# Performance work log

Hardware: AMD Instinct MI355X
Metric: run time of the kernel (lower is better)

## Reference

```python
import jax, jax.numpy as jnp
import numpy as np

D_MODEL = 1024
NUM_HEADS = 16
HEAD_DIM = D_MODEL // NUM_HEADS


def setup_inputs() -> dict:
    key = jax.random.key(0)
    k_x, k_qw, k_qb, k_pw, k_pb = jax.random.split(key, 5)
    x = jax.random.normal(k_x, (2, 2048, D_MODEL), dtype=jnp.float32)
    s = 1.0 / np.sqrt(D_MODEL)
    qkv_w = jax.random.uniform(k_qw, (3 * D_MODEL, D_MODEL), jnp.float32, -s, s)
    qkv_b = jax.random.uniform(k_qb, (3 * D_MODEL,), jnp.float32, -s, s)
    proj_w = jax.random.uniform(k_pw, (D_MODEL, D_MODEL), jnp.float32, -s, s)
    proj_b = jax.random.uniform(k_pb, (D_MODEL,), jnp.float32, -s, s)
    return {"x": x, "qkv_w": qkv_w, "qkv_b": qkv_b, "proj_w": proj_w, "proj_b": proj_b}


def reference(x, qkv_w, qkv_b, proj_w, proj_b):
    B, N, D = x.shape
    H, hd = NUM_HEADS, HEAD_DIM
    qkv = x @ qkv_w.T + qkv_b                     # [B, N, 3D]
    qkv = qkv.reshape(B, N, 3, H, hd).transpose(2, 0, 3, 1, 4)  # [3, B, H, N, hd]
    q, k, v = qkv[0], qkv[1], qkv[2]
    scale = hd ** -0.5
    attn = jnp.einsum('bhqd,bhkd->bhqk', q, k) * scale
    attn = jax.nn.softmax(attn, axis=-1)
    out = jnp.einsum('bhqk,bhkd->bhqd', attn, v)  # [B, H, N, hd]
    out = out.transpose(0, 2, 1, 3).reshape(B, N, D)
    return out @ proj_w.T + proj_b
```

## Files before the change

kernel.cpp:

```cpp
#include <hip/hip_runtime.h>
#include <hip/hip_bf16.h>
#include <math.h>

#define D_MODEL 1024
#define NHEAD 16
#define HDIM 64
#define BATCH 2
#define SEQ 2048
#define SCALE 0.125f

typedef unsigned short u16;
typedef __attribute__((ext_vector_type(8))) short bf16x8;
typedef __attribute__((ext_vector_type(4))) float f32x4;

__device__ __forceinline__ f32x4 mfma_bf16(bf16x8 a, bf16x8 b, f32x4 c) {
    return __builtin_amdgcn_mfma_f32_16x16x32_bf16(a, b, c, 0, 0, 0);
}
__device__ __forceinline__ void gload_lds16(const void* g, void* l) {
    __builtin_amdgcn_global_load_lds(
        (const __attribute__((address_space(1))) unsigned int*)g,
        (__attribute__((address_space(3))) unsigned int*)l, 16, 0, 0);
}
__device__ __forceinline__ u16 f2bf(float f) {
    unsigned u = __builtin_bit_cast(unsigned, f);
    return (u16)((u + 0x7FFFu + ((u >> 16) & 1u)) >> 16);
}

__global__ __launch_bounds__(256) void cvt_bf16(const float* __restrict__ in,
                                                u16* __restrict__ out, int n) {
    int i = (blockIdx.x * 256 + threadIdx.x) * 8;
    if (i >= n) return;
    float4 a = *(const float4*)&in[i];
    float4 b = *(const float4*)&in[i + 4];
    ushort4 o0 = { f2bf(a.x), f2bf(a.y), f2bf(a.z), f2bf(a.w) };
    ushort4 o1 = { f2bf(b.x), f2bf(b.y), f2bf(b.z), f2bf(b.w) };
    *(ushort4*)&out[i] = o0;
    *(ushort4*)&out[i + 4] = o1;
}

template<int MODE>
__global__ __launch_bounds__(256) void gemm_mfma(const u16* __restrict__ A,
                                                 const u16* __restrict__ W,
                                                 const float* __restrict__ bias,
                                                 float* __restrict__ outf,
                                                 u16* __restrict__ qw,
                                                 u16* __restrict__ kw,
                                                 u16* __restrict__ vtw)
{
    __shared__ u16 As[2][8192];
    __shared__ u16 Bs[2][8192];
    const int t = threadIdx.x, lane = t & 63, w = t >> 6;
    const int wr = w >> 1, wc = w & 1;
    const int lr = lane & 15, lk = lane >> 4;
    const int m0 = blockIdx.y * 128, n0 = blockIdx.x * 128;

    int srow[4], soff[4];
    #pragma unroll
    for (int i = 0; i < 4; ++i) {
        int p = (w * 4 + i) * 1024 + lane * 16;
        int row = p >> 7;
        srow[i] = row;
        soff[i] = ((p ^ ((row & 7) << 4)) & 127) >> 1;
    }

    f32x4 acc[4][4];
    #pragma unroll
    for (int i = 0; i < 4; ++i)
        #pragma unroll
        for (int j = 0; j < 4; ++j)
            #pragma unroll
            for (int r = 0; r < 4; ++r) acc[i][j][r] = 0.f;

    auto stage = [&](int buf, int k0) {
        #pragma unroll
        for (int i = 0; i < 4; ++i) {
            gload_lds16(&A[(size_t)(m0 + srow[i]) * 1024 + k0 + soff[i]],
                        &As[buf][(w * 4 + i) * 512]);
            gload_lds16(&W[(size_t)(n0 + srow[i]) * 1024 + k0 + soff[i]],
                        &Bs[buf][(w * 4 + i) * 512]);
        }
    };

    stage(0, 0);
    __syncthreads();

    for (int kt = 0; kt < 16; ++kt) {
        int buf = kt & 1;
        if (kt < 15) stage(buf ^ 1, (kt + 1) * 64);
        #pragma unroll
        for (int kk = 0; kk < 2; ++kk) {
            const int kb2 = (kk * 32 + lk * 8) * 2;
            bf16x8 am[4], bn[4];
            #pragma unroll
            for (int mf = 0; mf < 4; ++mf) {
                int row = wr * 64 + mf * 16 + lr;
                am[mf] = *(const bf16x8*)((const char*)As[buf] + row * 128 + (kb2 ^ ((row & 7) << 4)));
            }
            #pragma unroll
            for (int nf = 0; nf < 4; ++nf) {
                int row = wc * 64 + nf * 16 + lr;
                bn[nf] = *(const bf16x8*)((const char*)Bs[buf] + row * 128 + (kb2 ^ ((row & 7) << 4)));
            }
            #pragma unroll
            for (int mf = 0; mf < 4; ++mf)
                #pragma unroll
                for (int nf = 0; nf < 4; ++nf)
                    acc[mf][nf] = mfma_bf16(am[mf], bn[nf], acc[mf][nf]);
        }
        __syncthreads();
    }

    if (MODE == 0) {
        #pragma unroll
        for (int nf = 0; nf < 4; ++nf) {
            int n = n0 + wc * 64 + nf * 16 + lr;
            float bv = bias[n];
            #pragma unroll
            for (int mf = 0; mf < 4; ++mf) {
                int m = m0 + wr * 64 + mf * 16 + lk * 4;
                #pragma unroll
                for (int r = 0; r < 4; ++r)
                    outf[(size_t)(m + r) * 1024 + n] = acc[mf][nf][r] + bv;
            }
        }
    } else {
        #pragma unroll
        for (int nf = 0; nf < 4; ++nf) {
            int n = n0 + wc * 64 + nf * 16 + lr;
            int which = n >> 10, h = (n >> 6) & 15, d = n & 63;
            float bv = bias[n];
            #pragma unroll
            for (int mf = 0; mf < 4; ++mf) {
                int m = m0 + wr * 64 + mf * 16 + lk * 4;
                int b = m >> 11, sq = m & 2047;
                int bh = b * NHEAD + h;
                if (which == 2) {
                    ushort4 v4;
                    v4.x = f2bf(acc[mf][nf][0] + bv);
                    v4.y = f2bf(acc[mf][nf][1] + bv);
                    v4.z = f2bf(acc[mf][nf][2] + bv);
                    v4.w = f2bf(acc[mf][nf][3] + bv);
                    *(ushort4*)&vtw[((size_t)bh * 64 + d) * SEQ + sq] = v4;
                } else {
                    u16* dst = (which ? kw : qw) + ((size_t)bh * SEQ + sq) * 64 + d;
                    dst[0]   = f2bf(acc[mf][nf][0] + bv);
                    dst[64]  = f2bf(acc[mf][nf][1] + bv);
                    dst[128] = f2bf(acc[mf][nf][2] + bv);
                    dst[192] = f2bf(acc[mf][nf][3] + bv);
                }
            }
        }
    }
}

__global__ __launch_bounds__(256) void attn_mfma(const u16* __restrict__ qg,
                                                 const u16* __restrict__ kg,
                                                 const u16* __restrict__ vtg,
                                                 u16* __restrict__ og)
{
    __shared__ u16 Ks[2][4096];
    __shared__ u16 Vs[2][4096];
    __shared__ u16 Ps[4096];
    const int t = threadIdx.x, lane = t & 63, w = t >> 6;
    const int lr = lane & 15, lk = lane >> 4;
    const int q0 = blockIdx.x * 64;
    const int bh = blockIdx.y;
    const u16* Qbh = qg + (size_t)bh * SEQ * 64;
    const char* Kbytes = (const char*)(kg + (size_t)bh * SEQ * 64);
    const char* Vbytes = (const char*)(vtg + (size_t)bh * 64 * SEQ);

    bf16x8 qa[2];
    {
        const u16* qp = &Qbh[(size_t)(q0 + w * 16 + lr) * 64 + lk * 8];
        qa[0] = *(const bf16x8*)qp;
        qa[1] = *(const bf16x8*)(qp + 32);
    }

    int srow[2], soff[2];
    #pragma unroll
    for (int i = 0; i < 2; ++i) {
        int p = (w * 2 + i) * 1024 + lane * 16;
        int row = p >> 7;
        srow[i] = row;
        soff[i] = p ^ ((row & 7) << 4);
    }

    auto stage = [&](int buf, int tt) {
        #pragma unroll
        for (int i = 0; i < 2; ++i) {
            gload_lds16(Kbytes + (size_t)tt * 8192 + soff[i], &Ks[buf][(w * 2 + i) * 512]);
            gload_lds16(Vbytes + (size_t)srow[i] * (SEQ * 2) + tt * 128 + (soff[i] & 127),
                        &Vs[buf][(w * 2 + i) * 512]);
        }
    };

    f32x4 o[4];
    float mrow[4], lsum[4];
    #pragma unroll
    for (int fd = 0; fd < 4; ++fd)
        #pragma unroll
        for (int r = 0; r < 4; ++r) o[fd][r] = 0.f;
    #pragma unroll
    for (int r = 0; r < 4; ++r) { mrow[r] = -1e30f; lsum[r] = 0.f; }

    stage(0, 0);
    __syncthreads();

    for (int kt = 0; kt < SEQ / 64; ++kt) {
        int buf = kt & 1;
        if (kt < SEQ / 64 - 1) stage(buf ^ 1, kt + 1);

        f32x4 s[4];
        #pragma unroll
        for (int nf = 0; nf < 4; ++nf)
            #pragma unroll
            for (int r = 0; r < 4; ++r) s[nf][r] = 0.f;
        #pragma unroll
        for (int kk = 0; kk < 2; ++kk) {
            const int kb2 = (kk * 32 + lk * 8) * 2;
            #pragma unroll
            for (int nf = 0; nf < 4; ++nf) {
                int row = nf * 16 + lr;
                bf16x8 kb = *(const bf16x8*)((const char*)Ks[buf] + row * 128 + (kb2 ^ ((row & 7) << 4)));
                s[nf] = mfma_bf16(qa[kk], kb, s[nf]);
            }
        }

        float alpha[4];
        #pragma unroll
        for (int r = 0; r < 4; ++r) {
            float v0 = s[0][r] * SCALE, v1 = s[1][r] * SCALE,
                  v2 = s[2][r] * SCALE, v3 = s[3][r] * SCALE;
            float mx = fmaxf(fmaxf(v0, v1), fmaxf(v2, v3));
            #pragma unroll
            for (int o_ = 8; o_ >= 1; o_ >>= 1) mx = fmaxf(mx, __shfl_xor(mx, o_, 16));
            float mN = fmaxf(mrow[r], mx);
            float al = __expf(mrow[r] - mN);
            float p0 = __expf(v0 - mN), p1 = __expf(v1 - mN),
                  p2 = __expf(v2 - mN), p3 = __expf(v3 - mN);
            float rs = p0 + p1 + p2 + p3;
            #pragma unroll
            for (int o_ = 8; o_ >= 1; o_ >>= 1) rs += __shfl_xor(rs, o_, 16);
            lsum[r] = lsum[r] * al + rs;
            mrow[r] = mN;
            alpha[r] = al;
            const int qrow = w * 16 + lk * 4 + r;
            const int sw = (qrow & 7) << 4;
            char* pb = (char*)Ps + qrow * 128;
            *(u16*)(pb + (((0 * 16 + lr) * 2) ^ sw)) = f2bf(p0);
            *(u16*)(pb + (((1 * 16 + lr) * 2) ^ sw)) = f2bf(p1);
            *(u16*)(pb + (((2 * 16 + lr) * 2) ^ sw)) = f2bf(p2);
            *(u16*)(pb + (((3 * 16 + lr) * 2) ^ sw)) = f2bf(p3);
        }
        #pragma unroll
        for (int fd = 0; fd < 4; ++fd)
            #pragma unroll
            for (int r = 0; r < 4; ++r) o[fd][r] *= alpha[r];

        bf16x8 pa[2];
        {
            const int qrow = w * 16 + lr;
            const int sw = (qrow & 7) << 4;
            #pragma unroll
            for (int kk = 0; kk < 2; ++kk)
                pa[kk] = *(const bf16x8*)((const char*)Ps + qrow * 128 + (((kk * 32 + lk * 8) * 2) ^ sw));
        }
        #pragma unroll
        for (int kk = 0; kk < 2; ++kk) {
            const int kb2 = (kk * 32 + lk * 8) * 2;
            #pragma unroll
            for (int fd = 0; fd < 4; ++fd) {
                int row = fd * 16 + lr;
                bf16x8 vb = *(const bf16x8*)((const char*)Vs[buf] + row * 128 + (kb2 ^ ((row & 7) << 4)));
                o[fd] = mfma_bf16(pa[kk], vb, o[fd]);
            }
        }
        __syncthreads();
    }

    const int b = bh >> 4, h = bh & 15;
    #pragma unroll
    for (int r = 0; r < 4; ++r) {
        float inv = 1.0f / lsum[r];
        size_t orow = (size_t)(b * SEQ + q0 + w * 16 + lk * 4 + r) * D_MODEL;
        #pragma unroll
        for (int fd = 0; fd < 4; ++fd)
            og[orow + h * 64 + fd * 16 + lr] = f2bf(o[fd][r] * inv);
    }
}

extern "C" void kernel_launch(void* const* d_in, const int* in_sizes, int n_in,
                              void* d_out, int out_size, void* d_ws, size_t ws_size,
                              hipStream_t stream)
{
    const float* x      = (const float*)d_in[0];
    const float* qkv_w  = (const float*)d_in[1];
    const float* qkv_b  = (const float*)d_in[2];
    const float* proj_w = (const float*)d_in[3];
    const float* proj_b = (const float*)d_in[4];
    float* out = (float*)d_out;

    u16* xbf     = (u16*)d_ws;
    u16* qkvwbf  = xbf + (size_t)4 * 1024 * 1024;
    u16* projwbf = qkvwbf + (size_t)3 * 1024 * 1024;
    u16* qb      = projwbf + (size_t)1024 * 1024;
    u16* kb      = qb + (size_t)4 * 1024 * 1024;
    u16* vtb     = kb + (size_t)4 * 1024 * 1024;

    cvt_bf16<<<2048, 256, 0, stream>>>(x, xbf, 4 * 1024 * 1024);
    cvt_bf16<<<1536, 256, 0, stream>>>(qkv_w, qkvwbf, 3 * 1024 * 1024);
    cvt_bf16<<<512, 256, 0, stream>>>(proj_w, projwbf, 1024 * 1024);

    gemm_mfma<1><<<dim3(24, 32), 256, 0, stream>>>(xbf, qkvwbf, qkv_b, nullptr, qb, kb, vtb);
    attn_mfma<<<dim3(SEQ / 64, BATCH * NHEAD), 256, 0, stream>>>(qb, kb, vtb, xbf);
    gemm_mfma<0><<<dim3(8, 32), 256, 0, stream>>>(xbf, projwbf, proj_b, out, nullptr, nullptr, nullptr);
}
```

Baseline: 259.2 us.

## Compute transposed S in attention to keep P in registers, drop LDS round-trip

Swaps the MFMA operand order so each lane holds one query row's scores, which shrinks the row max and sum reductions to two cross-lane shuffles and removes per-row state arrays. P is packed to bf16 in registers and fed directly into 16x16x16 MFMAs against V, eliminating the shared-memory P buffer with its stores and reloads. The softmax scale is folded into Q inside the QKV GEMM epilogue, and output stores become vectorized. In exchange, PV uses twice as many smaller MFMA instructions.

```diff
diff --git a/kernel.cpp b/kernel.cpp
--- a/kernel.cpp
+++ b/kernel.cpp
@@ -7,14 +7,25 @@
 #define HDIM 64
 #define BATCH 2
 #define SEQ 2048
-#define SCALE 0.125f
+#define QSCALE 0.125f
 
 typedef unsigned short u16;
+typedef unsigned int u32;
 typedef __attribute__((ext_vector_type(8))) short bf16x8;
+typedef __attribute__((ext_vector_type(4))) short bf16x4;
+typedef __attribute__((ext_vector_type(2))) u32 u32x2;
 typedef __attribute__((ext_vector_type(4))) float f32x4;
 
 __device__ __forceinline__ f32x4 mfma_bf16(bf16x8 a, bf16x8 b, f32x4 c) {
     return __builtin_amdgcn_mfma_f32_16x16x32_bf16(a, b, c, 0, 0, 0);
+}
+__device__ __forceinline__ f32x4 mfma16(bf16x4 a, bf16x4 b, f32x4 c) {
+#if __has_builtin(__builtin_amdgcn_mfma_f32_16x16x16bf16_1k)
+    return __builtin_amdgcn_mfma_f32_16x16x16bf16_1k(a, b, c, 0, 0, 0);
+#else
+    asm volatile("v_mfma_f32_16x16x16_bf16 %0, %1, %2, %0" : "+v"(c) : "v"(a), "v"(b));
+    return c;
+#endif
 }
 __device__ __forceinline__ void gload_lds16(const void* g, void* l) {
     __builtin_amdgcn_global_load_lds(
@@ -24,6 +35,9 @@
 __device__ __forceinline__ u16 f2bf(float f) {
     unsigned u = __builtin_bit_cast(unsigned, f);
     return (u16)((u + 0x7FFFu + ((u >> 16) & 1u)) >> 16);
+}
+__device__ __forceinline__ u32 pack_bf16(float lo, float hi) {
+    return (u32)f2bf(lo) | ((u32)f2bf(hi) << 16);
 }
 
 __global__ __launch_bounds__(256) void cvt_bf16(const float* __restrict__ in,
@@ -141,12 +155,18 @@
                     v4.z = f2bf(acc[mf][nf][2] + bv);
                     v4.w = f2bf(acc[mf][nf][3] + bv);
                     *(ushort4*)&vtw[((size_t)bh * 64 + d) * SEQ + sq] = v4;
-                } else {
-                    u16* dst = (which ? kw : qw) + ((size_t)bh * SEQ + sq) * 64 + d;
+                } else if (which == 1) {
+                    u16* dst = kw + ((size_t)bh * SEQ + sq) * 64 + d;
                     dst[0]   = f2bf(acc[mf][nf][0] + bv);
                     dst[64]  = f2bf(acc[mf][nf][1] + bv);
                     dst[128] = f2bf(acc[mf][nf][2] + bv);
                     dst[192] = f2bf(acc[mf][nf][3] + bv);
+                } else {
+                    u16* dst = qw + ((size_t)bh * SEQ + sq) * 64 + d;
+                    dst[0]   = f2bf((acc[mf][nf][0] + bv) * QSCALE);
+                    dst[64]  = f2bf((acc[mf][nf][1] + bv) * QSCALE);
+                    dst[128] = f2bf((acc[mf][nf][2] + bv) * QSCALE);
+                    dst[192] = f2bf((acc[mf][nf][3] + bv) * QSCALE);
                 }
             }
         }
@@ -160,7 +180,6 @@
 {
     __shared__ u16 Ks[2][4096];
     __shared__ u16 Vs[2][4096];
-    __shared__ u16 Ps[4096];
     const int t = threadIdx.x, lane = t & 63, w = t >> 6;
     const int lr = lane & 15, lk = lane >> 4;
     const int q0 = blockIdx.x * 64;
@@ -195,13 +214,11 @@
     };
 
     f32x4 o[4];
-    float mrow[4], lsum[4];
     #pragma unroll
     for (int fd = 0; fd < 4; ++fd)
         #pragma unroll
         for (int r = 0; r < 4; ++r) o[fd][r] = 0.f;
-    #pragma unroll
-    for (int r = 0; r < 4; ++r) { mrow[r] = -1e30f; lsum[r] = 0.f; }
+    float mrow = -1e30f, lsum = 0.f;
 
     stage(0, 0);
     __syncthreads();
@@ -222,70 +239,65 @@
             for (int nf = 0; nf < 4; ++nf) {
                 int row = nf * 16 + lr;
                 bf16x8 kb = *(const bf16x8*)((const char*)Ks[buf] + row * 128 + (kb2 ^ ((row & 7) << 4)));
-                s[nf] = mfma_bf16(qa[kk], kb, s[nf]);
-            }
-        }
-
-        float alpha[4];
-        #pragma unroll
-        for (int r = 0; r < 4; ++r) {
-            float v0 = s[0][r] * SCALE, v1 = s[1][r] * SCALE,
-                  v2 = s[2][r] * SCALE, v3 = s[3][r] * SCALE;
-            float mx = fmaxf(fmaxf(v0, v1), fmaxf(v2, v3));
-            #pragma unroll
-            for (int o_ = 8; o_ >= 1; o_ >>= 1) mx = fmaxf(mx, __shfl_xor(mx, o_, 16));
-            float mN = fmaxf(mrow[r], mx);
-            float al = __expf(mrow[r] - mN);
-            float p0 = __expf(v0 - mN), p1 = __expf(v1 - mN),
-                  p2 = __expf(v2 - mN), p3 = __expf(v3 - mN);
-            float rs = p0 + p1 + p2 + p3;
-            #pragma unroll
-            for (int o_ = 8; o_ >= 1; o_ >>= 1) rs += __shfl_xor(rs, o_, 16);
-            lsum[r] = lsum[r] * al + rs;
-            mrow[r] = mN;
-            alpha[r] = al;
-            const int qrow = w * 16 + lk * 4 + r;
-            const int sw = (qrow & 7) << 4;
-            char* pb = (char*)Ps + qrow * 128;
-            *(u16*)(pb + (((0 * 16 + lr) * 2) ^ sw)) = f2bf(p0);
-            *(u16*)(pb + (((1 * 16 + lr) * 2) ^ sw)) = f2bf(p1);
-            *(u16*)(pb + (((2 * 16 + lr) * 2) ^ sw)) = f2bf(p2);
-            *(u16*)(pb + (((3 * 16 + lr) * 2) ^ sw)) = f2bf(p3);
-        }
+                s[nf] = mfma_bf16(kb, qa[kk], s[nf]);
+            }
+        }
+
+        float mx = s[0][0];
+        #pragma unroll
+        for (int nf = 0; nf < 4; ++nf)
+            #pragma unroll
+            for (int r = 0; r < 4; ++r) mx = fmaxf(mx, s[nf][r]);
+        mx = fmaxf(mx, __shfl_xor(mx, 16));
+        mx = fmaxf(mx, __shfl_xor(mx, 32));
+        const float mN = fmaxf(mrow, mx);
+        const float al = __expf(mrow - mN);
+        float p[4][4];
+        float rs = 0.f;
+        #pragma unroll
+        for (int nf = 0; nf < 4; ++nf) {
+            float t0 = __expf(s[nf][0] - mN), t1 = __expf(s[nf][1] - mN);
+            float t2 = __expf(s[nf][2] - mN), t3 = __expf(s[nf][3] - mN);
+            p[nf][0] = t0; p[nf][1] = t1; p[nf][2] = t2; p[nf][3] = t3;
+            rs += (t0 + t1) + (t2 + t3);
+        }
+        rs += __shfl_xor(rs, 16);
+        rs += __shfl_xor(rs, 32);
+        lsum = lsum * al + rs;
+        mrow = mN;
         #pragma unroll
         for (int fd = 0; fd < 4; ++fd)
             #pragma unroll
-            for (int r = 0; r < 4; ++r) o[fd][r] *= alpha[r];
-
-        bf16x8 pa[2];
-        {
-            const int qrow = w * 16 + lr;
-            const int sw = (qrow & 7) << 4;
-            #pragma unroll
-            for (int kk = 0; kk < 2; ++kk)
-                pa[kk] = *(const bf16x8*)((const char*)Ps + qrow * 128 + (((kk * 32 + lk * 8) * 2) ^ sw));
-        }
-        #pragma unroll
-        for (int kk = 0; kk < 2; ++kk) {
-            const int kb2 = (kk * 32 + lk * 8) * 2;
+            for (int r = 0; r < 4; ++r) o[fd][r] *= al;
+
+        #pragma unroll
+        for (int nf = 0; nf < 4; ++nf) {
+            u32x2 pw;
+            pw[0] = pack_bf16(p[nf][0], p[nf][1]);
+            pw[1] = pack_bf16(p[nf][2], p[nf][3]);
+            bf16x4 pb = __builtin_bit_cast(bf16x4, pw);
+            const int kvb = nf * 32 + lk * 8;
             #pragma unroll
             for (int fd = 0; fd < 4; ++fd) {
                 int row = fd * 16 + lr;
-                bf16x8 vb = *(const bf16x8*)((const char*)Vs[buf] + row * 128 + (kb2 ^ ((row & 7) << 4)));
-                o[fd] = mfma_bf16(pa[kk], vb, o[fd]);
+                bf16x4 vb = *(const bf16x4*)((const char*)Vs[buf] + row * 128 + (kvb ^ ((row & 7) << 4)));
+                o[fd] = mfma16(vb, pb, o[fd]);
             }
         }
         __syncthreads();
     }
 
     const int b = bh >> 4, h = bh & 15;
-    #pragma unroll
-    for (int r = 0; r < 4; ++r) {
-        float inv = 1.0f / lsum[r];
-        size_t orow = (size_t)(b * SEQ + q0 + w * 16 + lk * 4 + r) * D_MODEL;
-        #pragma unroll
-        for (int fd = 0; fd < 4; ++fd)
-            og[orow + h * 64 + fd * 16 + lr] = f2bf(o[fd][r] * inv);
+    const float inv = 1.0f / lsum;
+    const size_t orow = (size_t)(b * SEQ + q0 + w * 16 + lr) * D_MODEL;
+    #pragma unroll
+    for (int fd = 0; fd < 4; ++fd) {
+        ushort4 st;
+        st.x = f2bf(o[fd][0] * inv);
+        st.y = f2bf(o[fd][1] * inv);
+        st.z = f2bf(o[fd][2] * inv);
+        st.w = f2bf(o[fd][3] * inv);
+        *(ushort4*)&og[orow + h * 64 + fd * 16 + lk * 4] = st;
     }
 }
 
```

Measured after the change: 232.3 us. -10.4%, faster.
